# Performance work log

Measured on AMD Instinct MI355X. Metric: run time of the kernel, lower is better.

Reference implementation:

```python
import jax, jax.numpy as jnp
import numpy as np

B, C, H, W = 8, 256, 64, 64
D = C // 8  # 32


def setup_inputs() -> dict:
    key = jax.random.key(0)
    ks = jax.random.split(key, 6)
    s = 0.06  # ~1/sqrt(C): keeps q@k logits in a sane range so softmax is not one-hot
    x = jax.random.normal(ks[0], (B, C, H, W), dtype=jnp.float32)
    wq = jax.random.normal(ks[1], (D, C), dtype=jnp.float32) * s
    wk = jax.random.normal(ks[2], (D, C), dtype=jnp.float32) * s
    wv = jax.random.normal(ks[3], (D, C), dtype=jnp.float32) * s
    wo = jax.random.normal(ks[4], (C, D), dtype=jnp.float32) * s
    gamma = jax.random.uniform(ks[5], (1,), dtype=jnp.float32)
    return {"x": x, "wq": wq, "wk": wk, "wv": wv, "wo": wo, "gamma": gamma}


def reference(x, wq, wk, wv, wo, gamma):
    b, c, h, w = x.shape
    n = h * w
    xf = x.reshape(b, c, n)                          # [B,C,N]
    # 1x1 convs == channel matmuls
    q = jnp.einsum('dc,bcn->bnd', wq, xf)            # [B,N,D]
    k = jnp.einsum('dc,bcn->bdn', wk, xf)            # [B,D,N]
    v = jnp.einsum('dc,bcn->bdn', wv, xf)            # [B,D,N]
    # full NxN attention, softmax over keys (last axis), no 1/sqrt(d) scaling (as in source)
    attn = jax.nn.softmax(jnp.einsum('bnd,bdm->bnm', q, k), axis=-1)  # [B,N,N]
    out = jnp.einsum('bdm,bnm->bdn', v, attn)        # v @ attn^T -> [B,D,N]
    o = jnp.einsum('cd,bdn->bcn', wo, out).reshape(b, c, h, w)
    return o * gamma + x
```

## Files before the change

kernel.cpp:

```cpp
#include <hip/hip_runtime.h>
#include <hip/hip_bf16.h>
#include <hip/hip_fp16.h>


typedef _Float16 f16;
typedef f16 f16x8 __attribute__((ext_vector_type(8)));
typedef f16 f16x4 __attribute__((ext_vector_type(4)));
typedef __fp16 h16x2 __attribute__((ext_vector_type(2)));
typedef float f32x4 __attribute__((ext_vector_type(4)));

#define B_ 8
#define C_ 256
#define N_ 4096
#define D_ 32
#define LOG2E 1.44269504088896f

__device__ __forceinline__ float fexp2(float x) {
    float r;
    asm("v_exp_f32 %0, %1" : "=v"(r) : "v"(x));
    return r;
}

__global__ __launch_bounds__(256) void prep_kernel(
    const float* __restrict__ wq, const float* __restrict__ wk,
    const float* __restrict__ wv, const float* __restrict__ wo,
    const float* __restrict__ gamma,
    f16* __restrict__ whq, f16* __restrict__ whk,
    f16* __restrict__ whv, f16* __restrict__ woh)
{
    const int i = blockIdx.x * 256 + threadIdx.x;
    whq[i] = (f16)(wq[i] * LOG2E);
    whk[i] = (f16)wk[i];
    whv[i] = (f16)wv[i];
    woh[i] = (f16)(wo[i] * gamma[0]);
}

__global__ __launch_bounds__(256) void qkv2_kernel(
    const float* __restrict__ x, const f16* __restrict__ whq,
    const f16* __restrict__ whk, const f16* __restrict__ whv,
    f16* __restrict__ Q, f16* __restrict__ K, f16* __restrict__ Vt)
{
    const int lane = threadIdx.x & 63, wid = threadIdx.x >> 6;
    const int b = blockIdx.y;
    const int n0 = blockIdx.x * 64 + wid * 16;
    const int l15 = lane & 15, g = lane >> 4;
    const int n = n0 + l15;

    const float* xb = x + (size_t)b * C_ * N_ + n;
    f32x4 aq0 = {0.f, 0.f, 0.f, 0.f};
    f32x4 aq1 = aq0, ak0 = aq0, ak1 = aq0, av0 = aq0, av1 = aq0;

    #pragma unroll
    for (int ks = 0; ks < 8; ++ks) {
        const int c0 = ks * 32 + g * 8;
        float xr[8];
        #pragma unroll
        for (int j = 0; j < 8; ++j) xr[j] = xb[(size_t)(c0 + j) * N_];
        union { f16x8 v; h16x2 h[4]; } xf;
        #pragma unroll
        for (int j = 0; j < 4; ++j)
            xf.h[j] = __builtin_amdgcn_cvt_pkrtz(xr[2 * j], xr[2 * j + 1]);

        const int woff = l15 * 256 + c0;
        const f16x8 fq0 = *(const f16x8*)(whq + woff);
        const f16x8 fq1 = *(const f16x8*)(whq + woff + 16 * 256);
        const f16x8 fk0 = *(const f16x8*)(whk + woff);
        const f16x8 fk1 = *(const f16x8*)(whk + woff + 16 * 256);
        const f16x8 fv0 = *(const f16x8*)(whv + woff);
        const f16x8 fv1 = *(const f16x8*)(whv + woff + 16 * 256);

        aq0 = __builtin_amdgcn_mfma_f32_16x16x32_f16(fq0, xf.v, aq0, 0, 0, 0);
        aq1 = __builtin_amdgcn_mfma_f32_16x16x32_f16(fq1, xf.v, aq1, 0, 0, 0);
        ak0 = __builtin_amdgcn_mfma_f32_16x16x32_f16(fk0, xf.v, ak0, 0, 0, 0);
        ak1 = __builtin_amdgcn_mfma_f32_16x16x32_f16(fk1, xf.v, ak1, 0, 0, 0);
        av0 = __builtin_amdgcn_mfma_f32_16x16x32_f16(fv0, xf.v, av0, 0, 0, 0);
        av1 = __builtin_amdgcn_mfma_f32_16x16x32_f16(fv1, xf.v, av1, 0, 0, 0);
    }

    {
        f16x4 h0, h1;
        #pragma unroll
        for (int r = 0; r < 4; ++r) { h0[r] = (f16)aq0[r]; h1[r] = (f16)aq1[r]; }
        f16* qp = Q + ((size_t)b * N_ + n) * D_ + 4 * g;
        *(f16x4*)qp = h0; *(f16x4*)(qp + 16) = h1;
    }
    {
        f16x4 h0, h1;
        #pragma unroll
        for (int r = 0; r < 4; ++r) { h0[r] = (f16)ak0[r]; h1[r] = (f16)ak1[r]; }
        f16* kp = K + ((size_t)b * N_ + n) * D_ + 4 * g;
        *(f16x4*)kp = h0; *(f16x4*)(kp + 16) = h1;
    }
    {
        const int p = n & 31;
        const int cidx = (n & ~31) + 8 * ((p >> 2) & 3) + 4 * ((p >> 4) & 1) + (p & 3);
        f16* vb = Vt + ((size_t)b * D_ + 4 * g) * N_ + cidx;
        #pragma unroll
        for (int r = 0; r < 4; ++r) {
            vb[(size_t)r * N_]        = (f16)av0[r];
            vb[(size_t)(16 + r) * N_] = (f16)av1[r];
        }
    }
}

__global__ __launch_bounds__(256, 4) void flash_kernel(
    const f16* __restrict__ Qh, const f16* __restrict__ Kh,
    const f16* __restrict__ Vth, float* __restrict__ Opart,
    float* __restrict__ Ml, int kcnt, int kch)
{
    const int lane = threadIdx.x & 63;
    const int wid = threadIdx.x >> 6;
    const int b = blockIdx.x, kc = blockIdx.y, qt = blockIdx.z;
    const int q0 = qt * 128 + wid * 32;
    const int l15 = lane & 15, g = lane >> 4;

    const f16* qp = Qh + ((size_t)b * N_ + q0 + l15) * D_ + g * 8;
    const f16x8 qf0 = *(const f16x8*)qp;
    const f16x8 qf1 = *(const f16x8*)(qp + (size_t)16 * D_);

    const f16* kp = Kh + ((size_t)b * N_ + (size_t)kc * kch + l15) * D_ + g * 8;
    const f16* vp = Vth + ((size_t)b * D_ + l15) * N_ + (size_t)kc * kch + g * 8;

    f32x4 O00 = {0.f, 0.f, 0.f, 0.f};
    f32x4 O01 = O00, O10 = O00, O11 = O00;
    float m0 = -3e38f, m1 = -3e38f, l0 = 0.f, l1 = 0.f;
    const int NW = kch >> 5;

    f16x8 kf0 = *(const f16x8*)kp;
    f16x8 kf1 = *(const f16x8*)(kp + (size_t)16 * D_);
    f16x8 vf0 = *(const f16x8*)vp;
    f16x8 vf1 = *(const f16x8*)(vp + (size_t)16 * N_);

    for (int w = 0; w < NW; ++w) {
        const int wn = (w + 1 < NW) ? (w + 1) : w;
        const f16* kpn = kp + (size_t)wn * 32 * D_;
        const f16* vpn = vp + (size_t)wn * 32;
        const f16x8 kn0 = *(const f16x8*)kpn;
        const f16x8 kn1 = *(const f16x8*)(kpn + (size_t)16 * D_);
        const f16x8 vn0 = *(const f16x8*)vpn;
        const f16x8 vn1 = *(const f16x8*)(vpn + (size_t)16 * N_);

        const f32x4 z = {0.f, 0.f, 0.f, 0.f};
        __builtin_amdgcn_s_setprio(1);
        f32x4 s00 = __builtin_amdgcn_mfma_f32_16x16x32_f16(kf0, qf0, z, 0, 0, 0);
        f32x4 s01 = __builtin_amdgcn_mfma_f32_16x16x32_f16(kf1, qf0, z, 0, 0, 0);
        f32x4 s10 = __builtin_amdgcn_mfma_f32_16x16x32_f16(kf0, qf1, z, 0, 0, 0);
        f32x4 s11 = __builtin_amdgcn_mfma_f32_16x16x32_f16(kf1, qf1, z, 0, 0, 0);
        __builtin_amdgcn_s_setprio(0);

        union { f16x8 v; h16x2 h[4]; } pb0, pb1;
        {
            float mx = fmaxf(fmaxf(fmaxf(s00[0], s00[1]), fmaxf(s00[2], s00[3])),
                             fmaxf(fmaxf(s01[0], s01[1]), fmaxf(s01[2], s01[3])));
            mx = fmaxf(mx, __shfl_xor(mx, 16));
            mx = fmaxf(mx, __shfl_xor(mx, 32));
            if (__any(mx > m0 + 10.f)) {
                const float nm = fmaxf(m0, mx);
                const float f = fexp2(m0 - nm);
                m0 = nm; l0 *= f;
                #pragma unroll
                for (int r = 0; r < 4; ++r) { O00[r] *= f; O01[r] *= f; }
            }
            const float p0 = fexp2(s00[0] - m0), p1 = fexp2(s00[1] - m0);
            const float p2 = fexp2(s00[2] - m0), p3 = fexp2(s00[3] - m0);
            const float p4 = fexp2(s01[0] - m0), p5 = fexp2(s01[1] - m0);
            const float p6 = fexp2(s01[2] - m0), p7 = fexp2(s01[3] - m0);
            l0 += ((p0 + p1) + (p2 + p3)) + ((p4 + p5) + (p6 + p7));
            pb0.h[0] = __builtin_amdgcn_cvt_pkrtz(p0, p1);
            pb0.h[1] = __builtin_amdgcn_cvt_pkrtz(p2, p3);
            pb0.h[2] = __builtin_amdgcn_cvt_pkrtz(p4, p5);
            pb0.h[3] = __builtin_amdgcn_cvt_pkrtz(p6, p7);
        }
        {
            float mx = fmaxf(fmaxf(fmaxf(s10[0], s10[1]), fmaxf(s10[2], s10[3])),
                             fmaxf(fmaxf(s11[0], s11[1]), fmaxf(s11[2], s11[3])));
            mx = fmaxf(mx, __shfl_xor(mx, 16));
            mx = fmaxf(mx, __shfl_xor(mx, 32));
            if (__any(mx > m1 + 10.f)) {
                const float nm = fmaxf(m1, mx);
                const float f = fexp2(m1 - nm);
                m1 = nm; l1 *= f;
                #pragma unroll
                for (int r = 0; r < 4; ++r) { O10[r] *= f; O11[r] *= f; }
            }
            const float p0 = fexp2(s10[0] - m1), p1 = fexp2(s10[1] - m1);
            const float p2 = fexp2(s10[2] - m1), p3 = fexp2(s10[3] - m1);
            const float p4 = fexp2(s11[0] - m1), p5 = fexp2(s11[1] - m1);
            const float p6 = fexp2(s11[2] - m1), p7 = fexp2(s11[3] - m1);
            l1 += ((p0 + p1) + (p2 + p3)) + ((p4 + p5) + (p6 + p7));
            pb1.h[0] = __builtin_amdgcn_cvt_pkrtz(p0, p1);
            pb1.h[1] = __builtin_amdgcn_cvt_pkrtz(p2, p3);
            pb1.h[2] = __builtin_amdgcn_cvt_pkrtz(p4, p5);
            pb1.h[3] = __builtin_amdgcn_cvt_pkrtz(p6, p7);
        }

        __builtin_amdgcn_s_setprio(1);
        O00 = __builtin_amdgcn_mfma_f32_16x16x32_f16(vf0, pb0.v, O00, 0, 0, 0);
        O01 = __builtin_amdgcn_mfma_f32_16x16x32_f16(vf1, pb0.v, O01, 0, 0, 0);
        O10 = __builtin_amdgcn_mfma_f32_16x16x32_f16(vf0, pb1.v, O10, 0, 0, 0);
        O11 = __builtin_amdgcn_mfma_f32_16x16x32_f16(vf1, pb1.v, O11, 0, 0, 0);
        __builtin_amdgcn_s_setprio(0);

        kf0 = kn0; kf1 = kn1; vf0 = vn0; vf1 = vn1;
    }

    l0 += __shfl_xor(l0, 16); l0 += __shfl_xor(l0, 32);
    l1 += __shfl_xor(l1, 16); l1 += __shfl_xor(l1, 32);

    float* ob = Opart + (size_t)(b * kcnt + kc) * D_ * N_ + q0 + l15;
    #pragma unroll
    for (int r = 0; r < 4; ++r) {
        ob[(size_t)(g * 4 + r) * N_]           = O00[r];
        ob[(size_t)(16 + g * 4 + r) * N_]      = O01[r];
        ob[(size_t)(g * 4 + r) * N_ + 16]      = O10[r];
        ob[(size_t)(16 + g * 4 + r) * N_ + 16] = O11[r];
    }
    if (lane < 16) {
        float2* mp = (float2*)(Ml + ((size_t)(b * kcnt + kc) * N_ + q0 + l15) * 2);
        mp[0]  = make_float2(m0, l0);
        mp[16] = make_float2(m1, l1);
    }
}

__global__ __launch_bounds__(256) void merge2_kernel(
    const float* __restrict__ Opart, const float* __restrict__ Ml,
    const f16* __restrict__ woh, const float* __restrict__ x,
    float* __restrict__ out, int kcnt)
{
    const int lane = threadIdx.x & 63, wid = threadIdx.x >> 6;
    const int b = blockIdx.y;
    const int n0 = blockIdx.x * 64 + wid * 16;
    const int l15 = lane & 15, g = lane >> 4;
    const int n = n0 + l15;

    float mstar = -3e38f;
    for (int kc = 0; kc < kcnt; ++kc)
        mstar = fmaxf(mstar, Ml[(((size_t)b * kcnt + kc) * N_ + n) * 2]);

    float acc[8];
    #pragma unroll
    for (int j = 0; j < 8; ++j) acc[j] = 0.f;
    float lstar = 0.f;
    for (int kc = 0; kc < kcnt; ++kc) {
        const float2 ml = *(const float2*)(Ml + (((size_t)b * kcnt + kc) * N_ + n) * 2);
        const float wgt = fexp2(ml.x - mstar);
        lstar += wgt * ml.y;
        const float* op = Opart + (((size_t)b * kcnt + kc) * D_ + g * 8) * N_ + n;
        #pragma unroll
        for (int j = 0; j < 8; ++j) acc[j] += wgt * op[(size_t)j * N_];
    }
    const float inv = 1.0f / lstar;
    union { f16x8 v; h16x2 h[4]; } oc;
    #pragma unroll
    for (int j = 0; j < 4; ++j)
        oc.h[j] = __builtin_amdgcn_cvt_pkrtz(acc[2 * j] * inv, acc[2 * j + 1] * inv);

    const float* xb = x + (size_t)b * C_ * N_;
    float* ob = out + (size_t)b * C_ * N_;
    const f32x4 z = {0.f, 0.f, 0.f, 0.f};
    #pragma unroll
    for (int ct = 0; ct < 16; ++ct) {
        const f16x8 wf = *(const f16x8*)(woh + (ct * 16 + l15) * 32 + g * 8);
        const f32x4 o = __builtin_amdgcn_mfma_f32_16x16x32_f16(wf, oc.v, z, 0, 0, 0);
        #pragma unroll
        for (int r = 0; r < 4; ++r) {
            const size_t off = (size_t)(ct * 16 + 4 * g + r) * N_ + n;
            ob[off] = o[r] + xb[off];
        }
    }
}

extern "C" void kernel_launch(void* const* d_in, const int* in_sizes, int n_in,
                              void* d_out, int out_size, void* d_ws, size_t ws_size,
                              hipStream_t stream) {
    const float* x  = (const float*)d_in[0];
    const float* wq = (const float*)d_in[1];
    const float* wk = (const float*)d_in[2];
    const float* wv = (const float*)d_in[3];
    const float* wo = (const float*)d_in[4];
    const float* gm = (const float*)d_in[5];
    float* out = (float*)d_out;

    int kcnt = 8;
    while (kcnt > 1) {
        const size_t need = 65536
                          + 3 * (size_t)B_ * N_ * D_ * 2
                          + (size_t)kcnt * B_ * N_ * D_ * 4
                          + (size_t)kcnt * B_ * N_ * 2 * 4;
        if (need <= ws_size) break;
        kcnt >>= 1;
    }
    const int kch = N_ / kcnt;

    f16* whq = (f16*)d_ws;
    f16* whk = whq + 8192;
    f16* whv = whk + 8192;
    f16* woh = whv + 8192;
    f16* Qb  = woh + 8192;
    f16* Kb  = Qb + (size_t)B_ * N_ * D_;
    f16* Vtb = Kb + (size_t)B_ * N_ * D_;
    float* Opart = (float*)(Vtb + (size_t)B_ * N_ * D_);
    float* Mlb   = Opart + (size_t)kcnt * B_ * N_ * D_;

    prep_kernel<<<32, 256, 0, stream>>>(wq, wk, wv, wo, gm, whq, whk, whv, woh);
    qkv2_kernel<<<dim3(64, B_), 256, 0, stream>>>(x, whq, whk, whv, Qb, Kb, Vtb);
    flash_kernel<<<dim3(B_, kcnt, N_ / 128), 256, 0, stream>>>(Qb, Kb, Vtb, Opart, Mlb,
                                                               kcnt, kch);
    merge2_kernel<<<dim3(64, B_), 256, 0, stream>>>(Opart, Mlb, woh, x, out, kcnt);
}
```

Before: 168.4 us.

## Stage x through LDS, store partial outputs row-major, halve key split count

The QKV projection kernel now loads its 256x64 slab of x with coalesced float4 reads, converts it to fp16 in shared memory, and gathers the MFMA B-operands from LDS instead of issuing strided scalar global loads. The partial attention output is stored as [N][D] with 16-byte vector stores, and the merge kernel reads it back with vector loads. The split-K count drops from 8 to 4, which halves partial-output traffic and merge work but gives fewer attention blocks to fill the GPU. The added LDS buffer and barrier may lower occupancy in the projection kernel.

Result: slower. 173.6 us (+3.1%).

```diff
diff --git a/kernel.cpp b/kernel.cpp
--- a/kernel.cpp
+++ b/kernel.cpp
@@ -40,26 +40,37 @@
     const f16* __restrict__ whk, const f16* __restrict__ whv,
     f16* __restrict__ Q, f16* __restrict__ K, f16* __restrict__ Vt)
 {
-    const int lane = threadIdx.x & 63, wid = threadIdx.x >> 6;
+    __shared__ f16 xl[256][66];
+    const int tid = threadIdx.x;
+    const int lane = tid & 63, wid = tid >> 6;
     const int b = blockIdx.y;
-    const int n0 = blockIdx.x * 64 + wid * 16;
+    const int n0 = blockIdx.x * 64;
     const int l15 = lane & 15, g = lane >> 4;
-    const int n = n0 + l15;
-
-    const float* xb = x + (size_t)b * C_ * N_ + n;
+    const int nl = wid * 16 + l15;
+    const int n = n0 + nl;
+
+    {
+        const float* xb = x + (size_t)b * C_ * N_ + n0;
+        const int cb = tid >> 4, ncb = (tid & 15) * 4;
+        #pragma unroll
+        for (int i = 0; i < 16; ++i) {
+            const int c = i * 16 + cb;
+            const float4 xv = *(const float4*)(xb + (size_t)c * N_ + ncb);
+            *(h16x2*)&xl[c][ncb]     = __builtin_amdgcn_cvt_pkrtz(xv.x, xv.y);
+            *(h16x2*)&xl[c][ncb + 2] = __builtin_amdgcn_cvt_pkrtz(xv.z, xv.w);
+        }
+    }
+    __syncthreads();
+
     f32x4 aq0 = {0.f, 0.f, 0.f, 0.f};
     f32x4 aq1 = aq0, ak0 = aq0, ak1 = aq0, av0 = aq0, av1 = aq0;
 
     #pragma unroll
     for (int ks = 0; ks < 8; ++ks) {
         const int c0 = ks * 32 + g * 8;
-        float xr[8];
-        #pragma unroll
-        for (int j = 0; j < 8; ++j) xr[j] = xb[(size_t)(c0 + j) * N_];
-        union { f16x8 v; h16x2 h[4]; } xf;
-        #pragma unroll
-        for (int j = 0; j < 4; ++j)
-            xf.h[j] = __builtin_amdgcn_cvt_pkrtz(xr[2 * j], xr[2 * j + 1]);
+        union { f16x8 v; f16 e[8]; } xf;
+        #pragma unroll
+        for (int j = 0; j < 8; ++j) xf.e[j] = xl[c0 + j][nl];
 
         const int woff = l15 * 256 + c0;
         const f16x8 fq0 = *(const f16x8*)(whq + woff);
@@ -207,13 +218,12 @@
     l0 += __shfl_xor(l0, 16); l0 += __shfl_xor(l0, 32);
     l1 += __shfl_xor(l1, 16); l1 += __shfl_xor(l1, 32);
 
-    float* ob = Opart + (size_t)(b * kcnt + kc) * D_ * N_ + q0 + l15;
-    #pragma unroll
-    for (int r = 0; r < 4; ++r) {
-        ob[(size_t)(g * 4 + r) * N_]           = O00[r];
-        ob[(size_t)(16 + g * 4 + r) * N_]      = O01[r];
-        ob[(size_t)(g * 4 + r) * N_ + 16]      = O10[r];
-        ob[(size_t)(16 + g * 4 + r) * N_ + 16] = O11[r];
+    float* ob = Opart + ((size_t)(b * kcnt + kc) * N_ + q0) * D_;
+    {
+        *(f32x4*)(ob + (size_t)l15 * D_ + 4 * g) = O00;
+        *(f32x4*)(ob + (size_t)l15 * D_ + 16 + 4 * g) = O01;
+        *(f32x4*)(ob + (size_t)(16 + l15) * D_ + 4 * g) = O10;
+        *(f32x4*)(ob + (size_t)(16 + l15) * D_ + 16 + 4 * g) = O11;
     }
     if (lane < 16) {
         float2* mp = (float2*)(Ml + ((size_t)(b * kcnt + kc) * N_ + q0 + l15) * 2);
@@ -245,9 +255,11 @@
         const float2 ml = *(const float2*)(Ml + (((size_t)b * kcnt + kc) * N_ + n) * 2);
         const float wgt = fexp2(ml.x - mstar);
         lstar += wgt * ml.y;
-        const float* op = Opart + (((size_t)b * kcnt + kc) * D_ + g * 8) * N_ + n;
-        #pragma unroll
-        for (int j = 0; j < 8; ++j) acc[j] += wgt * op[(size_t)j * N_];
+        const float* op = Opart + ((size_t)(b * kcnt + kc) * N_ + n) * D_ + g * 8;
+        const f32x4 o0 = *(const f32x4*)op;
+        const f32x4 o1 = *(const f32x4*)(op + 4);
+        #pragma unroll
+        for (int j = 0; j < 4; ++j) { acc[j] += wgt * o0[j]; acc[4 + j] += wgt * o1[j]; }
     }
     const float inv = 1.0f / lstar;
     union { f16x8 v; h16x2 h[4]; } oc;
@@ -281,7 +293,7 @@
     const float* gm = (const float*)d_in[5];
     float* out = (float*)d_out;
 
-    int kcnt = 8;
+    int kcnt = 4;
     while (kcnt > 1) {
         const size_t need = 65536
                           + 3 * (size_t)B_ * N_ * D_ * 2
```
